# Performance work log

Measured on AMD Instinct MI355X. Metric: run time of the kernel, lower is better.

The kernel has to match this reference:

```python
import jax, jax.numpy as jnp
import numpy as np

GAP_JUNCTION_STRENGTH = 0.5
H = W = 4096

def _laplacian(v):
    # 5-point stencil; original code's boundary handling doubles the interior
    # neighbor, which is exactly reflect padding (mirror excluding the edge).
    p = jnp.pad(v, 1, mode='reflect')  # [H+2, W+2]
    return (p[2:, 1:-1] + p[:-2, 1:-1] + p[1:-1, 2:] + p[1:-1, :-2] - 4.0 * v)

def setup_inputs() -> dict:
    key = jax.random.key(0)
    k1, k2, k3, k4 = jax.random.split(key, 4)
    return {
        'voltage': jax.random.normal(k1, (H, W), dtype=jnp.float32),
        'sodium': jax.random.uniform(k2, (H, W), dtype=jnp.float32),
        'potassium': jax.random.uniform(k3, (H, W), dtype=jnp.float32),
        'calcium': jax.random.uniform(k4, (H, W), dtype=jnp.float32),
    }

def reference(voltage, sodium, potassium, calcium):
    lap = _laplacian(voltage)
    voltage_update = (GAP_JUNCTION_STRENGTH * lap
                      + 0.1 * sodium
                      - 0.05 * potassium
                      + 0.08 * calcium)
    new_voltage = jnp.tanh(voltage + 0.1 * voltage_update)
    new_sodium = sodium * 0.95 + 0.05 * jax.nn.relu(new_voltage)
    new_potassium = potassium * 0.95 + 0.05 * jax.nn.relu(-new_voltage)
    new_calcium = calcium * 0.95 + 0.05 * jnp.abs(new_voltage)
    return new_voltage, new_sodium, new_potassium, new_calcium
```

## Files before the change

### kernel.cpp

```cpp
#include <hip/hip_runtime.h>

#define HH 4096
#define WW 4096

__global__ __launch_bounds__(256) void bio_kernel(
    const float* __restrict__ v,
    const float* __restrict__ na,
    const float* __restrict__ kk,
    const float* __restrict__ ca,
    float* __restrict__ out)
{
    const int W4 = WW / 4;
    int tid = blockIdx.x * blockDim.x + threadIdx.x;
    if (tid >= HH * W4) return;
    int r  = tid / W4;
    int c4 = tid - r * W4;
    int c  = c4 * 4;
    long base = (long)r * WW + c;

    int rup = (r == 0)      ? 1      : r - 1;
    int rdn = (r == HH - 1) ? HH - 2 : r + 1;

    float4 vc = *(const float4*)(v + base);
    float4 vu = *(const float4*)(v + (long)rup * WW + c);
    float4 vd = *(const float4*)(v + (long)rdn * WW + c);
    float vl = (c == 0)       ? v[(long)r * WW + 1]      : v[base - 1];
    float vr = (c + 4 == WW)  ? v[(long)r * WW + WW - 2] : v[base + 4];

    float4 na4 = *(const float4*)(na + base);
    float4 k4  = *(const float4*)(kk + base);
    float4 ca4 = *(const float4*)(ca + base);

    float cv[4]  = {vc.x, vc.y, vc.z, vc.w};
    float uu[4]  = {vu.x, vu.y, vu.z, vu.w};
    float dd[4]  = {vd.x, vd.y, vd.z, vd.w};
    float lft[4] = {vl,   vc.x, vc.y, vc.z};
    float rgt[4] = {vc.y, vc.z, vc.w, vr};
    float nain[4] = {na4.x, na4.y, na4.z, na4.w};
    float kin[4]  = {k4.x,  k4.y,  k4.z,  k4.w};
    float cain[4] = {ca4.x, ca4.y, ca4.z, ca4.w};

    float ov[4], ona[4], okk[4], oca[4];
#pragma unroll
    for (int i = 0; i < 4; ++i) {
        float lap = uu[i] + dd[i] + lft[i] + rgt[i] - 4.0f * cv[i];
        float vupd = 0.5f * lap + 0.1f * nain[i] - 0.05f * kin[i] + 0.08f * cain[i];
        float nv = tanhf(cv[i] + 0.1f * vupd);
        ov[i]  = nv;
        ona[i] = nain[i] * 0.95f + 0.05f * fmaxf(nv, 0.0f);
        okk[i] = kin[i]  * 0.95f + 0.05f * fmaxf(-nv, 0.0f);
        oca[i] = cain[i] * 0.95f + 0.05f * fabsf(nv);
    }

    const long HW = (long)HH * WW;
    *(float4*)(out + base)          = make_float4(ov[0],  ov[1],  ov[2],  ov[3]);
    *(float4*)(out + HW + base)     = make_float4(ona[0], ona[1], ona[2], ona[3]);
    *(float4*)(out + 2 * HW + base) = make_float4(okk[0], okk[1], okk[2], okk[3]);
    *(float4*)(out + 3 * HW + base) = make_float4(oca[0], oca[1], oca[2], oca[3]);
}

extern "C" void kernel_launch(void* const* d_in, const int* in_sizes, int n_in,
                              void* d_out, int out_size, void* d_ws, size_t ws_size,
                              hipStream_t stream) {
    const float* v  = (const float*)d_in[0];
    const float* na = (const float*)d_in[1];
    const float* kk = (const float*)d_in[2];
    const float* ca = (const float*)d_in[3];
    float* out = (float*)d_out;

    int total = HH * (WW / 4);
    int block = 256;
    int grid = (total + block - 1) / block;
    bio_kernel<<<grid, block, 0, stream>>>(v, na, kk, ca, out);
}
```

Baseline: 109.5 us.

## Process two rows per thread, swizzle blocks across XCDs, use fast tanh

Each thread now computes a 2x4 tile instead of a 1x4 strip, so the vertical neighbour rows are shared between the two output rows. This cuts redundant voltage loads from three rows per output row to two. Block indices are remapped so each group of eight consecutive hardware block IDs covers contiguous chunks, which should improve L2 locality across XCDs. tanhf is replaced with an exp plus reciprocal formulation and 32-bit indexing is used, lowering ALU cost at some accuracy risk for large inputs.

```diff
diff --git a/kernel.cpp b/kernel.cpp
--- a/kernel.cpp
+++ b/kernel.cpp
@@ -2,6 +2,11 @@
 
 #define HH 4096
 #define WW 4096
+
+__device__ __forceinline__ float fast_tanh(float x) {
+    float e = __expf(2.0f * x);
+    return 1.0f - 2.0f * __builtin_amdgcn_rcpf(e + 1.0f);
+}
 
 __global__ __launch_bounds__(256) void bio_kernel(
     const float* __restrict__ v,
@@ -10,53 +15,73 @@
     const float* __restrict__ ca,
     float* __restrict__ out)
 {
-    const int W4 = WW / 4;
-    int tid = blockIdx.x * blockDim.x + threadIdx.x;
-    if (tid >= HH * W4) return;
-    int r  = tid / W4;
-    int c4 = tid - r * W4;
+    int bid   = blockIdx.x;
+    int chunk = gridDim.x >> 3;
+    int lb    = (bid & 7) * chunk + (bid >> 3);
+    int tid   = lb * 256 + (int)threadIdx.x;
+
+    int rp = tid >> 10;
+    int c4 = tid & 1023;
     int c  = c4 * 4;
-    long base = (long)r * WW + c;
+    int r0 = rp << 1;
+    int r1 = r0 + 1;
 
-    int rup = (r == 0)      ? 1      : r - 1;
-    int rdn = (r == HH - 1) ? HH - 2 : r + 1;
+    int b0 = r0 * WW + c;
+    int b1 = b0 + WW;
+    int rup = (r0 == 0)      ? 1      : r0 - 1;
+    int rdn = (r1 == HH - 1) ? HH - 2 : r1 + 1;
 
-    float4 vc = *(const float4*)(v + base);
-    float4 vu = *(const float4*)(v + (long)rup * WW + c);
-    float4 vd = *(const float4*)(v + (long)rdn * WW + c);
-    float vl = (c == 0)       ? v[(long)r * WW + 1]      : v[base - 1];
-    float vr = (c + 4 == WW)  ? v[(long)r * WW + WW - 2] : v[base + 4];
+    float4 vu = *(const float4*)(v + rup * WW + c);
+    float4 v0 = *(const float4*)(v + b0);
+    float4 v1 = *(const float4*)(v + b1);
+    float4 vd = *(const float4*)(v + rdn * WW + c);
 
-    float4 na4 = *(const float4*)(na + base);
-    float4 k4  = *(const float4*)(kk + base);
-    float4 ca4 = *(const float4*)(ca + base);
+    float l0, l1, re0, re1;
+    if (c == 0) { l0 = v[b0 + 1]; l1 = v[b1 + 1]; }
+    else        { l0 = v[b0 - 1]; l1 = v[b1 - 1]; }
+    if (c + 4 == WW) { re0 = v[b0 + 2]; re1 = v[b1 + 2]; }
+    else             { re0 = v[b0 + 4]; re1 = v[b1 + 4]; }
 
-    float cv[4]  = {vc.x, vc.y, vc.z, vc.w};
-    float uu[4]  = {vu.x, vu.y, vu.z, vu.w};
-    float dd[4]  = {vd.x, vd.y, vd.z, vd.w};
-    float lft[4] = {vl,   vc.x, vc.y, vc.z};
-    float rgt[4] = {vc.y, vc.z, vc.w, vr};
-    float nain[4] = {na4.x, na4.y, na4.z, na4.w};
-    float kin[4]  = {k4.x,  k4.y,  k4.z,  k4.w};
-    float cain[4] = {ca4.x, ca4.y, ca4.z, ca4.w};
+    float4 na0 = *(const float4*)(na + b0);
+    float4 na1 = *(const float4*)(na + b1);
+    float4 k0  = *(const float4*)(kk + b0);
+    float4 k1  = *(const float4*)(kk + b1);
+    float4 ca0 = *(const float4*)(ca + b0);
+    float4 ca1 = *(const float4*)(ca + b1);
 
-    float ov[4], ona[4], okk[4], oca[4];
+    float cv[2][4] = {{v0.x, v0.y, v0.z, v0.w}, {v1.x, v1.y, v1.z, v1.w}};
+    float up[2][4] = {{vu.x, vu.y, vu.z, vu.w}, {v0.x, v0.y, v0.z, v0.w}};
+    float dn[2][4] = {{v1.x, v1.y, v1.z, v1.w}, {vd.x, vd.y, vd.z, vd.w}};
+    float lf[2][4] = {{l0, v0.x, v0.y, v0.z}, {l1, v1.x, v1.y, v1.z}};
+    float rt[2][4] = {{v0.y, v0.z, v0.w, re0}, {v1.y, v1.z, v1.w, re1}};
+    float nai[2][4] = {{na0.x, na0.y, na0.z, na0.w}, {na1.x, na1.y, na1.z, na1.w}};
+    float ki[2][4]  = {{k0.x, k0.y, k0.z, k0.w},     {k1.x, k1.y, k1.z, k1.w}};
+    float cai[2][4] = {{ca0.x, ca0.y, ca0.z, ca0.w}, {ca1.x, ca1.y, ca1.z, ca1.w}};
+
+    const int HW = HH * WW;
+    float ov[2][4], ona[2][4], okk[2][4], oca[2][4];
 #pragma unroll
-    for (int i = 0; i < 4; ++i) {
-        float lap = uu[i] + dd[i] + lft[i] + rgt[i] - 4.0f * cv[i];
-        float vupd = 0.5f * lap + 0.1f * nain[i] - 0.05f * kin[i] + 0.08f * cain[i];
-        float nv = tanhf(cv[i] + 0.1f * vupd);
-        ov[i]  = nv;
-        ona[i] = nain[i] * 0.95f + 0.05f * fmaxf(nv, 0.0f);
-        okk[i] = kin[i]  * 0.95f + 0.05f * fmaxf(-nv, 0.0f);
-        oca[i] = cain[i] * 0.95f + 0.05f * fabsf(nv);
+    for (int i = 0; i < 2; ++i) {
+#pragma unroll
+        for (int j = 0; j < 4; ++j) {
+            float lap  = up[i][j] + dn[i][j] + lf[i][j] + rt[i][j] - 4.0f * cv[i][j];
+            float vupd = 0.5f * lap + 0.1f * nai[i][j] - 0.05f * ki[i][j] + 0.08f * cai[i][j];
+            float nv   = fast_tanh(cv[i][j] + 0.1f * vupd);
+            ov[i][j]  = nv;
+            ona[i][j] = nai[i][j] * 0.95f + 0.05f * fmaxf(nv, 0.0f);
+            okk[i][j] = ki[i][j]  * 0.95f + 0.05f * fmaxf(-nv, 0.0f);
+            oca[i][j] = cai[i][j] * 0.95f + 0.05f * fabsf(nv);
+        }
     }
 
-    const long HW = (long)HH * WW;
-    *(float4*)(out + base)          = make_float4(ov[0],  ov[1],  ov[2],  ov[3]);
-    *(float4*)(out + HW + base)     = make_float4(ona[0], ona[1], ona[2], ona[3]);
-    *(float4*)(out + 2 * HW + base) = make_float4(okk[0], okk[1], okk[2], okk[3]);
-    *(float4*)(out + 3 * HW + base) = make_float4(oca[0], oca[1], oca[2], oca[3]);
+#pragma unroll
+    for (int i = 0; i < 2; ++i) {
+        int b = (i == 0) ? b0 : b1;
+        *(float4*)(out + b)          = make_float4(ov[i][0],  ov[i][1],  ov[i][2],  ov[i][3]);
+        *(float4*)(out + HW + b)     = make_float4(ona[i][0], ona[i][1], ona[i][2], ona[i][3]);
+        *(float4*)(out + 2 * HW + b) = make_float4(okk[i][0], okk[i][1], okk[i][2], okk[i][3]);
+        *(float4*)(out + 3 * HW + b) = make_float4(oca[i][0], oca[i][1], oca[i][2], oca[i][3]);
+    }
 }
 
 extern "C" void kernel_launch(void* const* d_in, const int* in_sizes, int n_in,
@@ -68,8 +93,8 @@
     const float* ca = (const float*)d_in[3];
     float* out = (float*)d_out;
 
-    int total = HH * (WW / 4);
+    int total = (HH / 2) * (WW / 4);
     int block = 256;
-    int grid = (total + block - 1) / block;
+    int grid  = total / block;
     bio_kernel<<<grid, block, 0, stream>>>(v, na, kk, ca, out);
 }
```

Result: slower. 118.6 us (+8.3%).
